# Kernel optimization log

Hardware: AMD Instinct MI355X
Metric: run time of the kernel (lower is better)

## Reference

```python
import jax, jax.numpy as jnp
import numpy as np

B, S = 32, 4096
HID, MEM, ATT = 512, 512, 512


def setup_inputs() -> dict:
    key = jax.random.key(0)
    k1, k2, k3, k4, k5, k6, k7 = jax.random.split(key, 7)
    scale_h = 1.0 / np.sqrt(HID)
    scale_m = 1.0 / np.sqrt(MEM)
    scale_a = 1.0 / np.sqrt(ATT)
    return {
        "hidden": jax.random.normal(k1, (B, HID), dtype=jnp.float32),
        "memory": jax.random.normal(k2, (B, S, MEM), dtype=jnp.float32),
        "mem_pad": jnp.zeros((B, S), dtype=jnp.bool_),
        "coverage": jax.random.uniform(k3, (B, S), dtype=jnp.float32),
        # params stored as (in, out) so x @ W == torch Linear(x)
        "W_h": jax.random.uniform(k4, (HID, ATT), minval=-scale_h, maxval=scale_h, dtype=jnp.float32),
        "W_m": jax.random.uniform(k5, (MEM, ATT), minval=-scale_m, maxval=scale_m, dtype=jnp.float32),
        "W_c": jax.random.uniform(k6, (ATT,), minval=-1.0, maxval=1.0, dtype=jnp.float32),
        "v": jax.random.uniform(k7, (ATT,), minval=-scale_a, maxval=scale_a, dtype=jnp.float32),
    }


def reference(hidden, memory, mem_pad, coverage, W_h, W_m, W_c, v):
    h = hidden @ W_h                                   # (B, A)
    m = jnp.einsum('bsd,da->bsa', memory, W_m)         # (B, S, A)
    c_feat = coverage[..., None] * W_c                 # (B, S, A) ; Linear(1->A) == scalar * weight row
    score = jnp.einsum('bsa,a->bs', jnp.tanh(h[:, None, :] + m + c_feat), v)  # (B, S)
    score = jnp.where(mem_pad, -jnp.inf, score)
    attn_weights = jax.nn.softmax(score, axis=-1)      # (B, S)
    context = jnp.einsum('bs,bsd->bd', attn_weights, memory)  # (B, D)
    return context, attn_weights
```

## Files before the change

kernel.cpp:

```cpp
#include <hip/hip_runtime.h>
#include <hip/hip_bf16.h>
#include <math.h>

#define BB 32
#define SS 4096
#define DMEM 512
#define DATT 512

typedef short short8 __attribute__((ext_vector_type(8)));
typedef float floatx4 __attribute__((ext_vector_type(4)));

__device__ inline short f2bf(float x) {
    unsigned u = __float_as_uint(x);
    unsigned r = (u + 0x7fffu + ((u >> 16) & 1u)) >> 16;
    return (short)(r & 0xffffu);
}

__device__ inline float fast_tanh(float x) {
    float e = __expf(2.0f * x);
    float r = __builtin_amdgcn_rcpf(e + 1.0f);
    return __builtin_fmaf(-2.0f, r, 1.0f);
}

__device__ inline void gld_lds16(const void* g, void* l) {
    __builtin_amdgcn_global_load_lds(
        (const __attribute__((address_space(1))) unsigned int*)g,
        (__attribute__((address_space(3))) unsigned int*)l, 16, 0, 0);
}


__global__ void prep_wt_kernel(const float* __restrict__ Wm, short* __restrict__ Wt) {
    const int n0 = blockIdx.x * 32;
    const int k0 = blockIdx.y * 32;
    const int t = threadIdx.x;
    const int r = t >> 5, c = t & 31;
    __shared__ float lds[32 * 33];
#pragma unroll
    for (int j = 0; j < 4; ++j) {
        int kk = r + j * 8;
        lds[kk * 33 + c] = Wm[(size_t)(k0 + kk) * 512 + n0 + c];
    }
    __syncthreads();
#pragma unroll
    for (int j = 0; j < 4; ++j) {
        int nn = r + j * 8;
        Wt[(size_t)(n0 + nn) * 512 + k0 + c] = f2bf(lds[c * 33 + nn]);
    }
}

__global__ void prep_h_kernel(const float* __restrict__ hidden, const float* __restrict__ Wh,
                              float* __restrict__ h) {
    const int b = blockIdx.x;
    const int n = blockIdx.y * 256 + threadIdx.x;
    const int kc = blockIdx.z;
    float acc = 0.f;
#pragma unroll 8
    for (int k = kc * 128; k < kc * 128 + 128; ++k)
        acc += hidden[b * 512 + k] * Wh[(size_t)k * 512 + n];
    atomicAdd(&h[b * 512 + n], acc);
}


__global__ __launch_bounds__(1024, 4)
void fused_kernel(const float* __restrict__ memory,
                  const float* __restrict__ coverage,
                  const unsigned char* __restrict__ pad,
                  const short* __restrict__ Wt,
                  const float* __restrict__ h,
                  const float* __restrict__ Wc,
                  const float* __restrict__ v,
                  float* __restrict__ pOut,
                  float* __restrict__ mWS,
                  float* __restrict__ lWS,
                  float* __restrict__ ctxPart) {
    const int blk = blockIdx.x;
    const int b = blk >> 5;
    const int st = blk & 31;
    const int s0 = st * 128;

    const int tid = threadIdx.x;
    const int lane = tid & 63;
    const int wave = tid >> 6;
    const int wm = wave & 1;
    const int wn = wave >> 1;
    const int col = lane & 15;
    const int q = lane >> 4;

    __shared__ __align__(16) char smem[87560];
    char* bufB0 = smem;
    char* bufB1 = smem + 32768;
    char* bufA0 = smem + 65536;
    char* bufA1 = smem + 73728;
    float* covS   = (float*)(smem + 81920);
    float* sred   = (float*)(smem + 82432);
    float* scoreS = (float*)(smem + 86528);
    float* pS     = (float*)(smem + 87040);
    float* mlS    = (float*)(smem + 87552);
    float4* red4  = (float4*)smem;

    if (tid < 128) covS[tid] = coverage[(size_t)b * SS + s0 + tid];

    const float4* gA4 = (const float4*)(memory + ((size_t)b * SS + s0) * 512);
    const char* gB = (const char*)Wt;

    const int arow = tid >> 3, al8 = tid & 7;
    const int aoff = arow * 64 + (((al8 >> 1) ^ ((arow >> 1) & 3)) << 4) + ((al8 & 1) << 3);

    float4 apfA;

    floatx4 acc[4][4];
#pragma unroll
    for (int mi = 0; mi < 4; ++mi)
#pragma unroll
        for (int ni = 0; ni < 4; ++ni)
            acc[mi][ni] = (floatx4){0.f, 0.f, 0.f, 0.f};

    apfA = gA4[(size_t)arow * 128 + al8];
#pragma unroll
    for (int it = 0; it < 2; ++it) {
        int ci = it * 1024 + tid;
        int row = ci >> 2;
        int gch = (ci & 3) ^ ((row >> 1) & 3);
        gld_lds16(gB + (size_t)row * 1024 + gch * 16,
                  bufB0 + it * 16384 + wave * 1024);
    }
    __builtin_amdgcn_sched_barrier(0);
    {
        union { __hip_bfloat162 h2; unsigned u; } p0, p1;
        p0.h2 = __float22bfloat162_rn(make_float2(apfA.x, apfA.y));
        p1.h2 = __float22bfloat162_rn(make_float2(apfA.z, apfA.w));
        uint2 w; w.x = p0.u; w.y = p1.u;
        *(uint2*)(bufA0 + aoff) = w;
    }
    apfA = gA4[(size_t)arow * 128 + 8 + al8];
    __builtin_amdgcn_sched_barrier(0);
    asm volatile("s_waitcnt vmcnt(1)" ::: "memory");
    asm volatile("s_waitcnt lgkmcnt(0)" ::: "memory");
    __builtin_amdgcn_s_barrier();

#pragma unroll
    for (int kt = 0; kt < 16; ++kt) {
        if (kt < 15) {
            char* ldsB = ((kt + 1) & 1) ? bufB1 : bufB0;
#pragma unroll
            for (int it = 0; it < 2; ++it) {
                int ci = it * 1024 + tid;
                int row = ci >> 2;
                int gch = (ci & 3) ^ ((row >> 1) & 3);
                gld_lds16(gB + (size_t)row * 1024 + (kt + 1) * 64 + gch * 16,
                          ldsB + it * 16384 + wave * 1024);
            }
            __builtin_amdgcn_sched_barrier(0);
        }

        const char* abase = (kt & 1) ? bufA1 : bufA0;
        const char* bbase = (kt & 1) ? bufB1 : bufB0;
        short8 af[4], bf[4];
#pragma unroll
        for (int mi = 0; mi < 4; ++mi) {
            int row = wm * 64 + mi * 16 + col;
            af[mi] = *(const short8*)(abase + row * 64 + ((q ^ ((row >> 1) & 3)) << 4));
        }
#pragma unroll
        for (int ni = 0; ni < 4; ++ni) {
            int row = wn * 64 + ni * 16 + col;
            bf[ni] = *(const short8*)(bbase + row * 64 + ((q ^ ((row >> 1) & 3)) << 4));
        }

        if (kt < 15) {
            union { __hip_bfloat162 h2; unsigned u; } p0, p1;
            p0.h2 = __float22bfloat162_rn(make_float2(apfA.x, apfA.y));
            p1.h2 = __float22bfloat162_rn(make_float2(apfA.z, apfA.w));
            uint2 w; w.x = p0.u; w.y = p1.u;
            char* dst = ((kt + 1) & 1) ? bufA1 : bufA0;
            *(uint2*)(dst + aoff) = w;
            if (kt < 14)
                apfA = gA4[(size_t)arow * 128 + (kt + 2) * 8 + al8];
        }

#pragma unroll
        for (int mi = 0; mi < 4; ++mi)
#pragma unroll
            for (int ni = 0; ni < 4; ++ni)
                acc[mi][ni] = __builtin_amdgcn_mfma_f32_16x16x32_bf16(af[mi], bf[ni], acc[mi][ni], 0, 0, 0);

        if (kt < 15) {
            __builtin_amdgcn_sched_barrier(0);
            if (kt < 14) {
                asm volatile("s_waitcnt vmcnt(1)" ::: "memory");
            } else {
                asm volatile("s_waitcnt vmcnt(0)" ::: "memory");
            }
            asm volatile("s_waitcnt lgkmcnt(0)" ::: "memory");
            __builtin_amdgcn_s_barrier();
        }
    }

    __syncthreads();

    float hv[4], wcv[4], vv[4];
#pragma unroll
    for (int ni = 0; ni < 4; ++ni) {
        int n = wn * 64 + ni * 16 + col;
        hv[ni] = h[b * 512 + n];
        wcv[ni] = Wc[n];
        vv[ni] = v[n];
    }
    float rowAcc[4][4];
#pragma unroll
    for (int mi = 0; mi < 4; ++mi)
#pragma unroll
        for (int r = 0; r < 4; ++r)
            rowAcc[mi][r] = 0.f;
#pragma unroll
    for (int mi = 0; mi < 4; ++mi) {
#pragma unroll
        for (int r = 0; r < 4; ++r) {
            float cv = covS[wm * 64 + mi * 16 + q * 4 + r];
#pragma unroll
            for (int ni = 0; ni < 4; ++ni) {
                float val = acc[mi][ni][r] + hv[ni] + cv * wcv[ni];
                rowAcc[mi][r] += fast_tanh(val) * vv[ni];
            }
        }
    }
#pragma unroll
    for (int off = 1; off < 16; off <<= 1)
#pragma unroll
        for (int mi = 0; mi < 4; ++mi)
#pragma unroll
            for (int r = 0; r < 4; ++r)
                rowAcc[mi][r] += __shfl_xor(rowAcc[mi][r], off, 64);

    if (col == 0) {
#pragma unroll
        for (int mi = 0; mi < 4; ++mi)
#pragma unroll
            for (int r = 0; r < 4; ++r)
                sred[wn * 128 + wm * 64 + mi * 16 + q * 4 + r] = rowAcc[mi][r];
    }
    __syncthreads();

    if (tid < 128) {
        float sc = 0.f;
#pragma unroll
        for (int w = 0; w < 8; ++w) sc += sred[w * 128 + tid];
        if (pad[(size_t)b * SS + s0 + tid]) sc = -INFINITY;
        scoreS[tid] = sc;
    }
    __syncthreads();
    if (tid < 64) {
        float mx = fmaxf(scoreS[tid], scoreS[tid + 64]);
#pragma unroll
        for (int off = 32; off >= 1; off >>= 1) mx = fmaxf(mx, __shfl_xor(mx, off, 64));
        if (tid == 0) mlS[0] = mx;
    }
    __syncthreads();
    const float mtile = mlS[0];
    if (tid < 128) pS[tid] = __expf(scoreS[tid] - mtile);
    __syncthreads();
    if (tid < 64) {
        float sm = pS[tid] + pS[tid + 64];
#pragma unroll
        for (int off = 32; off >= 1; off >>= 1) sm += __shfl_xor(sm, off, 64);
        if (tid == 0) mlS[1] = sm;
    }
    __syncthreads();

    if (tid < 128) pOut[(size_t)b * SS + s0 + tid] = pS[tid];
    if (tid == 0) {
        mWS[b * 32 + st] = mtile;
        lWS[b * 32 + st] = mlS[1];
    }

    const int sg = tid >> 7;
    const int dc = tid & 127;
    const float4* m4 = (const float4*)(memory + ((size_t)b * SS + s0) * 512);
    float4 a4 = {0.f, 0.f, 0.f, 0.f};
#pragma unroll 8
    for (int i = 0; i < 16; ++i) {
        int s = sg * 16 + i;
        float w = pS[s];
        float4 f = m4[(size_t)s * 128 + dc];
        a4.x += w * f.x; a4.y += w * f.y; a4.z += w * f.z; a4.w += w * f.w;
    }
    red4[sg * 128 + dc] = a4;
    __syncthreads();
    if (tid < 128) {
        float4 o = {0.f, 0.f, 0.f, 0.f};
#pragma unroll
        for (int g2 = 0; g2 < 8; ++g2) {
            float4 r = red4[g2 * 128 + tid];
            o.x += r.x; o.y += r.y; o.z += r.z; o.w += r.w;
        }
        ((float4*)(ctxPart + ((size_t)(b * 32 + st)) * 512))[tid] = o;
    }
}

__global__ __launch_bounds__(512)
void combine_kernel(const float* __restrict__ mWS,
                    const float* __restrict__ lWS,
                    const float* __restrict__ ctxPart,
                    float* __restrict__ ctx,
                    float* __restrict__ attn) {
    const int b = blockIdx.x;
    const int tid = threadIdx.x;
    __shared__ float scaleS[32];
    __shared__ float gS[2];

    if (tid < 64) {
        float mv = (tid < 32) ? mWS[b * 32 + tid] : -INFINITY;
#pragma unroll
        for (int off = 32; off >= 1; off >>= 1) mv = fmaxf(mv, __shfl_xor(mv, off, 64));
        if (tid == 0) gS[0] = mv;
    }
    __syncthreads();
    const float gmax = gS[0];
    if (tid < 64) {
        float sc = 0.f, lv = 0.f;
        if (tid < 32) {
            sc = __expf(mWS[b * 32 + tid] - gmax);
            scaleS[tid] = sc;
            lv = lWS[b * 32 + tid] * sc;
        }
#pragma unroll
        for (int off = 32; off >= 1; off >>= 1) lv += __shfl_xor(lv, off, 64);
        if (tid == 0) gS[1] = lv;
    }
    __syncthreads();
    const float inv = 1.0f / gS[1];

    float facc = 0.f;
#pragma unroll 8
    for (int st = 0; st < 32; ++st)
        facc += ctxPart[((size_t)(b * 32 + st)) * 512 + tid] * scaleS[st];
    ctx[b * 512 + tid] = facc * inv;

#pragma unroll
    for (int j = 0; j < 8; ++j) {
        size_t idx = (size_t)b * SS + j * 512 + tid;
        attn[idx] = attn[idx] * scaleS[(j * 512 + tid) >> 7] * inv;
    }
}

extern "C" void kernel_launch(void* const* d_in, const int* in_sizes, int n_in,
                              void* d_out, int out_size, void* d_ws, size_t ws_size,
                              hipStream_t stream) {
    (void)in_sizes; (void)n_in; (void)out_size; (void)ws_size;
    const float* hidden   = (const float*)d_in[0];
    const float* memory   = (const float*)d_in[1];
    const unsigned char* mem_pad = (const unsigned char*)d_in[2];
    const float* coverage = (const float*)d_in[3];
    const float* Wh       = (const float*)d_in[4];
    const float* Wm       = (const float*)d_in[5];
    const float* Wc       = (const float*)d_in[6];
    const float* v        = (const float*)d_in[7];

    char* ws = (char*)d_ws;
    short* Wt      = (short*)ws;
    float* h       = (float*)(ws + 512 * 1024);
    float* mWS     = (float*)(ws + 576 * 1024);
    float* lWS     = (float*)(ws + 580 * 1024);
    float* ctxPart = (float*)(ws + 584 * 1024);

    float* ctx  = (float*)d_out;
    float* attn = (float*)d_out + BB * 512;

    hipMemsetAsync(h, 0, BB * 512 * sizeof(float), stream);
    prep_wt_kernel<<<dim3(16, 16), dim3(256), 0, stream>>>(Wm, Wt);
    prep_h_kernel<<<dim3(32, 2, 4), dim3(256), 0, stream>>>(hidden, Wh, h);
    fused_kernel<<<dim3(BB * 32), dim3(1024), 0, stream>>>(
        memory, coverage, mem_pad, Wt, h, Wc, v, attn, mWS, lWS, ctxPart);
    combine_kernel<<<dim3(BB), dim3(512), 0, stream>>>(mWS, lWS, ctxPart, ctx, attn);
}
```

Measured before the change: 453.8 us.

## Triple-buffer W tiles with two-ahead prefetch and merge prep kernels

```diff
diff --git a/kernel.cpp b/kernel.cpp
--- a/kernel.cpp
+++ b/kernel.cpp
@@ -29,35 +29,37 @@
 }
 
 
-__global__ void prep_wt_kernel(const float* __restrict__ Wm, short* __restrict__ Wt) {
-    const int n0 = blockIdx.x * 32;
-    const int k0 = blockIdx.y * 32;
+__global__ __launch_bounds__(512)
+void prep_kernel(const float* __restrict__ Wm, short* __restrict__ Wt,
+                 const float* __restrict__ hidden, const float* __restrict__ Wh,
+                 float* __restrict__ h) {
+    const int blk = blockIdx.x;
     const int t = threadIdx.x;
-    const int r = t >> 5, c = t & 31;
     __shared__ float lds[32 * 33];
-#pragma unroll
-    for (int j = 0; j < 4; ++j) {
-        int kk = r + j * 8;
-        lds[kk * 33 + c] = Wm[(size_t)(k0 + kk) * 512 + n0 + c];
-    }
-    __syncthreads();
-#pragma unroll
-    for (int j = 0; j < 4; ++j) {
-        int nn = r + j * 8;
-        Wt[(size_t)(n0 + nn) * 512 + k0 + c] = f2bf(lds[c * 33 + nn]);
-    }
-}
-
-__global__ void prep_h_kernel(const float* __restrict__ hidden, const float* __restrict__ Wh,
-                              float* __restrict__ h) {
-    const int b = blockIdx.x;
-    const int n = blockIdx.y * 256 + threadIdx.x;
-    const int kc = blockIdx.z;
-    float acc = 0.f;
+    if (blk < 256) {
+        const int n0 = (blk & 15) * 32;
+        const int k0 = (blk >> 4) * 32;
+        const int r = t >> 5, c = t & 31;
+#pragma unroll
+        for (int j = 0; j < 2; ++j) {
+            int kk = r + j * 16;
+            lds[kk * 33 + c] = Wm[(size_t)(k0 + kk) * 512 + n0 + c];
+        }
+        __syncthreads();
+#pragma unroll
+        for (int j = 0; j < 2; ++j) {
+            int nn = r + j * 16;
+            Wt[(size_t)(n0 + nn) * 512 + k0 + c] = f2bf(lds[c * 33 + nn]);
+        }
+    } else {
+        const int b = blk - 256;
+        const int n = t;
+        float acc = 0.f;
 #pragma unroll 8
-    for (int k = kc * 128; k < kc * 128 + 128; ++k)
-        acc += hidden[b * 512 + k] * Wh[(size_t)k * 512 + n];
-    atomicAdd(&h[b * 512 + n], acc);
+        for (int k = 0; k < 512; ++k)
+            acc += hidden[b * 512 + k] * Wh[(size_t)k * 512 + n];
+        h[b * 512 + n] = acc;
+    }
 }
 
 
@@ -86,16 +88,14 @@
     const int col = lane & 15;
     const int q = lane >> 4;
 
-    __shared__ __align__(16) char smem[87560];
-    char* bufB0 = smem;
-    char* bufB1 = smem + 32768;
-    char* bufA0 = smem + 65536;
-    char* bufA1 = smem + 73728;
-    float* covS   = (float*)(smem + 81920);
-    float* sred   = (float*)(smem + 82432);
-    float* scoreS = (float*)(smem + 86528);
-    float* pS     = (float*)(smem + 87040);
-    float* mlS    = (float*)(smem + 87552);
+    __shared__ __align__(16) char smem[120328];
+    char* bufBp[3] = { smem, smem + 32768, smem + 65536 };
+    char* bufAp[2] = { smem + 98304, smem + 106496 };
+    float* covS   = (float*)(smem + 114688);
+    float* sred   = (float*)(smem + 115200);
+    float* scoreS = (float*)(smem + 119296);
+    float* pS     = (float*)(smem + 119808);
+    float* mlS    = (float*)(smem + 120320);
     float4* red4  = (float4*)smem;
 
     if (tid < 128) covS[tid] = coverage[(size_t)b * SS + s0 + tid];
@@ -117,12 +117,15 @@
 
     apfA = gA4[(size_t)arow * 128 + al8];
 #pragma unroll
-    for (int it = 0; it < 2; ++it) {
-        int ci = it * 1024 + tid;
-        int row = ci >> 2;
-        int gch = (ci & 3) ^ ((row >> 1) & 3);
-        gld_lds16(gB + (size_t)row * 1024 + gch * 16,
-                  bufB0 + it * 16384 + wave * 1024);
+    for (int t2 = 0; t2 < 2; ++t2) {
+#pragma unroll
+        for (int it = 0; it < 2; ++it) {
+            int ci = it * 1024 + tid;
+            int row = ci >> 2;
+            int gch = (ci & 3) ^ ((row >> 1) & 3);
+            gld_lds16(gB + (size_t)row * 1024 + t2 * 64 + gch * 16,
+                      bufBp[t2] + it * 16384 + wave * 1024);
+        }
     }
     __builtin_amdgcn_sched_barrier(0);
     {
@@ -130,31 +133,31 @@
         p0.h2 = __float22bfloat162_rn(make_float2(apfA.x, apfA.y));
         p1.h2 = __float22bfloat162_rn(make_float2(apfA.z, apfA.w));
         uint2 w; w.x = p0.u; w.y = p1.u;
-        *(uint2*)(bufA0 + aoff) = w;
+        *(uint2*)(bufAp[0] + aoff) = w;
     }
     apfA = gA4[(size_t)arow * 128 + 8 + al8];
     __builtin_amdgcn_sched_barrier(0);
-    asm volatile("s_waitcnt vmcnt(1)" ::: "memory");
+    asm volatile("s_waitcnt vmcnt(3)" ::: "memory");
     asm volatile("s_waitcnt lgkmcnt(0)" ::: "memory");
     __builtin_amdgcn_s_barrier();
 
 #pragma unroll
     for (int kt = 0; kt < 16; ++kt) {
-        if (kt < 15) {
-            char* ldsB = ((kt + 1) & 1) ? bufB1 : bufB0;
+        if (kt < 14) {
+            char* ldsB = bufBp[(kt + 2) % 3];
 #pragma unroll
             for (int it = 0; it < 2; ++it) {
                 int ci = it * 1024 + tid;
                 int row = ci >> 2;
                 int gch = (ci & 3) ^ ((row >> 1) & 3);
-                gld_lds16(gB + (size_t)row * 1024 + (kt + 1) * 64 + gch * 16,
+                gld_lds16(gB + (size_t)row * 1024 + (kt + 2) * 64 + gch * 16,
                           ldsB + it * 16384 + wave * 1024);
             }
             __builtin_amdgcn_sched_barrier(0);
         }
 
-        const char* abase = (kt & 1) ? bufA1 : bufA0;
-        const char* bbase = (kt & 1) ? bufB1 : bufB0;
+        const char* abase = bufAp[kt & 1];
+        const char* bbase = bufBp[kt % 3];
         short8 af[4], bf[4];
 #pragma unroll
         for (int mi = 0; mi < 4; ++mi) {
@@ -172,8 +175,7 @@
             p0.h2 = __float22bfloat162_rn(make_float2(apfA.x, apfA.y));
             p1.h2 = __float22bfloat162_rn(make_float2(apfA.z, apfA.w));
             uint2 w; w.x = p0.u; w.y = p1.u;
-            char* dst = ((kt + 1) & 1) ? bufA1 : bufA0;
-            *(uint2*)(dst + aoff) = w;
+            *(uint2*)(bufAp[(kt + 1) & 1] + aoff) = w;
             if (kt < 14)
                 apfA = gA4[(size_t)arow * 128 + (kt + 2) * 8 + al8];
         }
@@ -187,7 +189,7 @@
         if (kt < 15) {
             __builtin_amdgcn_sched_barrier(0);
             if (kt < 14) {
-                asm volatile("s_waitcnt vmcnt(1)" ::: "memory");
+                asm volatile("s_waitcnt vmcnt(3)" ::: "memory");
             } else {
                 asm volatile("s_waitcnt vmcnt(0)" ::: "memory");
             }
@@ -366,9 +368,7 @@
     float* ctx  = (float*)d_out;
     float* attn = (float*)d_out + BB * 512;
 
-    hipMemsetAsync(h, 0, BB * 512 * sizeof(float), stream);
-    prep_wt_kernel<<<dim3(16, 16), dim3(256), 0, stream>>>(Wm, Wt);
-    prep_h_kernel<<<dim3(32, 2, 4), dim3(256), 0, stream>>>(hidden, Wh, h);
+    prep_kernel<<<dim3(288), dim3(512), 0, stream>>>(Wm, Wt, hidden, Wh, h);
     fused_kernel<<<dim3(BB * 32), dim3(1024), 0, stream>>>(
         memory, coverage, mem_pad, Wt, h, Wc, v, attn, mWS, lWS, ctxPart);
     combine_kernel<<<dim3(BB), dim3(512), 0, stream>>>(mWS, lWS, ctxPart, ctx, attn);
```

Measured after the change: 481.6 us. 6.1% more time.
